# Kernel tuning notes

Hardware: AMD Instinct MI355X
Metric: run time of the kernel (lower is better)

Reference implementation:

```python
import jax, jax.numpy as jnp
import numpy as np

TEMPERATURE = 8.0  # sqrt(d_k)
WINDOW = 2
GATE_THRESH = 0.5
NEG_INF = -1e30


def setup_inputs() -> dict:
    key = jax.random.key(0)
    k1, k2, k3, k4 = jax.random.split(key, 4)
    BH, L, D = 32, 2048, 64
    return {
        "q": jax.random.normal(k1, (BH, L, D), dtype=jnp.float32),
        "k": jax.random.normal(k2, (BH, L, D), dtype=jnp.float32),
        "v": jax.random.normal(k3, (BH, L, D), dtype=jnp.float32),
        "gate_w": jax.random.normal(k4, (1, D), dtype=jnp.float32) * 0.1,
        "gate_b": jnp.zeros((1,), dtype=jnp.float32),
    }


def reference(q, k, v, gate_w, gate_b):
    # q,k: [BH, L, D]; v: [BH, L, Dv]
    BH, Lq, D = q.shape
    Lk = k.shape[1]
    attn = jnp.einsum("bqd,bkd->bqk", q, k) / TEMPERATURE  # [BH, Lq, Lk]
    # per-query gate: if sigmoid(linear(q)) <= thresh, restrict to sliding window
    gate = jax.nn.sigmoid(jnp.einsum("bqd,od->bqo", q, gate_w) + gate_b) > GATE_THRESH  # [BH,Lq,1]
    i = jnp.arange(Lq)[:, None]
    j = jnp.arange(Lk)[None, :]
    window_ok = jnp.abs(i - j) <= WINDOW  # [Lq, Lk]; equals left=max(0,i-W), right=min(Lk,i+W+1)
    allowed = gate | window_ok[None, :, :]  # gate True -> full attention
    attn = jnp.where(allowed, attn, NEG_INF)
    attn = jax.nn.softmax(attn, axis=2)
    # dropout omitted (eval mode)
    out = jnp.einsum("bqk,bkd->bqd", attn, v)
    return out, attn
```

## Files before the change

kernel.cpp:

```cpp
#include <hip/hip_runtime.h>


typedef short bf16x8 __attribute__((ext_vector_type(8)));
typedef float f32x4  __attribute__((ext_vector_type(4)));

#define LSEQ 2048
#define DDIM 64
#define PB_STRIDE 36

__device__ __forceinline__ unsigned short f2bf(float x) {
    unsigned int u = __float_as_uint(x);
    u += 0x7FFFu + ((u >> 16) & 1u);
    return (unsigned short)(u >> 16);
}

__device__ __forceinline__ unsigned int pk2f(float a, float b) {
    return (unsigned int)f2bf(a) | ((unsigned int)f2bf(b) << 16);
}

__device__ __forceinline__ unsigned int pk2u(unsigned short a, unsigned short b) {
    return (unsigned int)a | ((unsigned int)b << 16);
}

__device__ __forceinline__ float pick5(int jj, float e0, float e1, float e2,
                                       float e3, float e4) {
    float r = 0.f;
    r = (jj == 0) ? e0 : r;
    r = (jj == 1) ? e1 : r;
    r = (jj == 2) ? e2 : r;
    r = (jj == 3) ? e3 : r;
    r = (jj == 4) ? e4 : r;
    return r;
}

__global__ __launch_bounds__(256)
void dsa_prep(const float* __restrict__ K, const float* __restrict__ V,
              unsigned short* __restrict__ Kb, unsigned short* __restrict__ Vt)
{
    const int bh  = blockIdx.x >> 5;
    const int k0  = (blockIdx.x & 31) << 6;
    const int tid = threadIdx.x;
    __shared__ unsigned short tileT[64][73];

    const int key = tid >> 2;
    const int d0  = (tid & 3) << 4;
    const float* srcK = K + ((size_t)bh * LSEQ + k0 + key) * DDIM + d0;
    const float* srcV = V + ((size_t)bh * LSEQ + k0 + key) * DDIM + d0;
    {
        uint4 w0, w1;
        w0.x = pk2f(srcK[0],  srcK[1]);  w0.y = pk2f(srcK[2],  srcK[3]);
        w0.z = pk2f(srcK[4],  srcK[5]);  w0.w = pk2f(srcK[6],  srcK[7]);
        w1.x = pk2f(srcK[8],  srcK[9]);  w1.y = pk2f(srcK[10], srcK[11]);
        w1.z = pk2f(srcK[12], srcK[13]); w1.w = pk2f(srcK[14], srcK[15]);
        unsigned short* dst = Kb + ((size_t)bh * LSEQ + k0 + key) * DDIM + d0;
        *(uint4*)(dst)     = w0;
        *(uint4*)(dst + 8) = w1;
    }
    #pragma unroll
    for (int j = 0; j < 16; ++j) tileT[d0 + j][key] = f2bf(srcV[j]);
    __syncthreads();
    {
        const int d   = tid >> 2;
        const int kk0 = (tid & 3) << 4;
        uint4 w0, w1;
        w0.x = pk2u(tileT[d][kk0 + 0],  tileT[d][kk0 + 1]);
        w0.y = pk2u(tileT[d][kk0 + 2],  tileT[d][kk0 + 3]);
        w0.z = pk2u(tileT[d][kk0 + 4],  tileT[d][kk0 + 5]);
        w0.w = pk2u(tileT[d][kk0 + 6],  tileT[d][kk0 + 7]);
        w1.x = pk2u(tileT[d][kk0 + 8],  tileT[d][kk0 + 9]);
        w1.y = pk2u(tileT[d][kk0 + 10], tileT[d][kk0 + 11]);
        w1.z = pk2u(tileT[d][kk0 + 12], tileT[d][kk0 + 13]);
        w1.w = pk2u(tileT[d][kk0 + 14], tileT[d][kk0 + 15]);
        unsigned short* dst = Vt + (size_t)bh * DDIM * LSEQ + (size_t)d * LSEQ + k0 + kk0;
        *(uint4*)(dst)     = w0;
        *(uint4*)(dst + 8) = w1;
    }
}

__global__ __launch_bounds__(256, 4)
void dsa_main(const float* __restrict__ Q,
              const unsigned short* __restrict__ Kb,
              const unsigned short* __restrict__ Vt,
              const float* __restrict__ K32,
              const float* __restrict__ V32,
              const float* __restrict__ GW,
              const float* __restrict__ GB,
              float* __restrict__ OUT,
              float* __restrict__ ATT)
{
    __shared__ float Pbuf[4][16 * PB_STRIDE];
    __shared__ int   sidx[64];
    __shared__ int   gShared;

    const int bx   = blockIdx.x;
    const int bh   = bx >> 5;
    const int q0   = (bx & 31) << 6;
    const int tid  = threadIdx.x;
    const int wave = tid >> 6;
    const int lane = tid & 63;
    const int m16  = lane & 15;
    const int quad = lane >> 4;

    const float* qb = Q + ((size_t)bh * LSEQ + q0) * DDIM;

    if (wave == 0) {
        const float* qr = qb + lane * DDIM;
        float a = 0.f;
        #pragma unroll 8
        for (int d = 0; d < DDIM; ++d) a += qr[d] * GW[d];
        a += GB[0];
        const bool gt = (a > 0.f);
        const unsigned long long b = __ballot(gt);
        const int below = __popcll(b & ((1ull << lane) - 1ull));
        const int g     = __popcll(b);
        const int pos   = gt ? below : (g + (lane - below));
        sidx[pos] = lane;
        if (lane == 0) gShared = g;
    }
    __syncthreads();
    const int g = gShared;
    const int T = (g + 15) >> 4;

    if (wave < T) {
        const unsigned short* kbb = Kb + (size_t)bh * LSEQ * DDIM;
        const unsigned short* vtb = Vt + (size_t)bh * DDIM * LSEQ;
        const int  myIdx = (wave << 4) + m16;
        const bool valid = myIdx < g;
        const int  srow  = sidx[valid ? myIdx : (g - 1)];

        bf16x8 qfrag[2];
        {
            const float* qr = qb + srow * DDIM + (quad << 3);
            #pragma unroll
            for (int db = 0; db < 2; ++db) {
                const float* p = qr + db * 32;
                bf16x8 f;
                #pragma unroll
                for (int j = 0; j < 8; ++j) f[j] = (short)f2bf(p[j]);
                qfrag[db] = f;
            }
        }

        const unsigned short* kp0 = kbb + (size_t)m16 * DDIM + (quad << 3);

        float lsum[4] = {0.f, 0.f, 0.f, 0.f};
        bf16x8 c0 = *(const bf16x8*)(kp0);
        bf16x8 c1 = *(const bf16x8*)(kp0 + 32);
        bf16x8 c2 = *(const bf16x8*)(kp0 + 16 * DDIM);
        bf16x8 c3 = *(const bf16x8*)(kp0 + 16 * DDIM + 32);
        for (int kt = 0; kt < 64; ++kt) {
            const unsigned short* np = kp0 + (size_t)(((kt + 1) & 63) * 32) * DDIM;
            bf16x8 n0 = *(const bf16x8*)(np);
            bf16x8 n1 = *(const bf16x8*)(np + 32);
            bf16x8 n2 = *(const bf16x8*)(np + 16 * DDIM);
            bf16x8 n3 = *(const bf16x8*)(np + 16 * DDIM + 32);
            f32x4 a0 = {0.f, 0.f, 0.f, 0.f}, a1 = {0.f, 0.f, 0.f, 0.f};
            a0 = __builtin_amdgcn_mfma_f32_16x16x32_bf16(qfrag[0], c0, a0, 0, 0, 0);
            a0 = __builtin_amdgcn_mfma_f32_16x16x32_bf16(qfrag[1], c1, a0, 0, 0, 0);
            a1 = __builtin_amdgcn_mfma_f32_16x16x32_bf16(qfrag[0], c2, a1, 0, 0, 0);
            a1 = __builtin_amdgcn_mfma_f32_16x16x32_bf16(qfrag[1], c3, a1, 0, 0, 0);
            #pragma unroll
            for (int r = 0; r < 4; ++r)
                lsum[r] += __expf(a0[r] * 0.125f) + __expf(a1[r] * 0.125f);
            c0 = n0; c1 = n1; c2 = n2; c3 = n3;
        }
        float inv[4];
        #pragma unroll
        for (int r = 0; r < 4; ++r) {
            float x = lsum[r];
            x += __shfl_xor(x, 1); x += __shfl_xor(x, 2);
            x += __shfl_xor(x, 4); x += __shfl_xor(x, 8);
            inv[r] = 1.0f / x;
        }

        f32x4 oacc[4];
        #pragma unroll
        for (int dt = 0; dt < 4; ++dt) oacc[dt] = (f32x4){0.f, 0.f, 0.f, 0.f};
        float* pw  = &Pbuf[wave][0];
        float* ap0 = ATT + ((size_t)(bh * LSEQ + q0 + srow)) * LSEQ + (quad << 3);
        const unsigned short* vp0 = vtb + (size_t)m16 * LSEQ + (quad << 3);

        for (int kt = 0; kt < 64; ++kt) {
            const unsigned short* kp = kp0 + (size_t)(kt * 32) * DDIM;
            bf16x8 k0 = *(const bf16x8*)(kp);
            bf16x8 k1 = *(const bf16x8*)(kp + 32);
            bf16x8 k2 = *(const bf16x8*)(kp + 16 * DDIM);
            bf16x8 k3 = *(const bf16x8*)(kp + 16 * DDIM + 32);
            const unsigned short* vp = vp0 + kt * 32;
            bf16x8 v0 = *(const bf16x8*)(vp);
            bf16x8 v1 = *(const bf16x8*)(vp + 16 * LSEQ);
            bf16x8 v2 = *(const bf16x8*)(vp + 32 * LSEQ);
            bf16x8 v3 = *(const bf16x8*)(vp + 48 * LSEQ);

            f32x4 a0 = {0.f, 0.f, 0.f, 0.f}, a1 = {0.f, 0.f, 0.f, 0.f};
            a0 = __builtin_amdgcn_mfma_f32_16x16x32_bf16(qfrag[0], k0, a0, 0, 0, 0);
            a0 = __builtin_amdgcn_mfma_f32_16x16x32_bf16(qfrag[1], k1, a0, 0, 0, 0);
            a1 = __builtin_amdgcn_mfma_f32_16x16x32_bf16(qfrag[0], k2, a1, 0, 0, 0);
            a1 = __builtin_amdgcn_mfma_f32_16x16x32_bf16(qfrag[1], k3, a1, 0, 0, 0);

            #pragma unroll
            for (int r = 0; r < 4; ++r) {
                const int prow = (quad << 2) + r;
                pw[prow * PB_STRIDE + m16]      = __expf(a0[r] * 0.125f) * inv[r];
                pw[prow * PB_STRIDE + 16 + m16] = __expf(a1[r] * 0.125f) * inv[r];
            }
            const float* prd = pw + m16 * PB_STRIDE + (quad << 3);
            f32x4 p0 = *(const f32x4*)(prd);
            f32x4 p1 = *(const f32x4*)(prd + 4);
            if (valid) {
                float* ap = ap0 + kt * 32;
                *(f32x4*)(ap)     = p0;
                *(f32x4*)(ap + 4) = p1;
            }
            bf16x8 pf;
            #pragma unroll
            for (int j = 0; j < 4; ++j) {
                pf[j]     = (short)f2bf(p0[j]);
                pf[4 + j] = (short)f2bf(p1[j]);
            }
            oacc[0] = __builtin_amdgcn_mfma_f32_16x16x32_bf16(pf, v0, oacc[0], 0, 0, 0);
            oacc[1] = __builtin_amdgcn_mfma_f32_16x16x32_bf16(pf, v1, oacc[1], 0, 0, 0);
            oacc[2] = __builtin_amdgcn_mfma_f32_16x16x32_bf16(pf, v2, oacc[2], 0, 0, 0);
            oacc[3] = __builtin_amdgcn_mfma_f32_16x16x32_bf16(pf, v3, oacc[3], 0, 0, 0);
        }
        #pragma unroll
        for (int r = 0; r < 4; ++r) {
            const int idx = (wave << 4) + (quad << 2) + r;
            if (idx < g) {
                const int orow = sidx[idx];
                float* ob = OUT + ((size_t)(bh * LSEQ + q0 + orow)) * DDIM + m16;
                ob[0]  = oacc[0][r];
                ob[16] = oacc[1][r];
                ob[32] = oacc[2][r];
                ob[48] = oacc[3][r];
            }
        }
    }

    const int nw    = 64 - g;
    const int nww   = (T < 4) ? (4 - T) : 4;
    const int wslot = (T < 4) ? (wave - T) : wave;
    if (wslot >= 0 && nw > 0) {
        for (int ii = wslot; ii < nw; ii += nww) {
            const int row = sidx[g + ii];
            const int i   = q0 + row;
            const float qd = qb[row * DDIM + lane];

            float e[5];
            float denom = 0.f;
            #pragma unroll
            for (int jj = 0; jj < 5; ++jj) {
                const int  j  = i - 2 + jj;
                const bool ok = (j >= 0) && (j < LSEQ);
                const int  jc = ok ? j : 0;
                float t = qd * K32[((size_t)bh * LSEQ + jc) * DDIM + lane];
                t += __shfl_xor(t, 1);  t += __shfl_xor(t, 2);
                t += __shfl_xor(t, 4);  t += __shfl_xor(t, 8);
                t += __shfl_xor(t, 16); t += __shfl_xor(t, 32);
                const float ee = ok ? __expf(t * 0.125f) : 0.f;
                e[jj] = ee;
                denom += ee;
            }
            const float invd = 1.f / denom;
            #pragma unroll
            for (int jj = 0; jj < 5; ++jj) e[jj] *= invd;

            float o = 0.f;
            #pragma unroll
            for (int jj = 0; jj < 5; ++jj) {
                const int  j  = i - 2 + jj;
                const int  jc = (j >= 0 && j < LSEQ) ? j : 0;
                o += e[jj] * V32[((size_t)bh * LSEQ + jc) * DDIM + lane];
            }
            OUT[((size_t)(bh * LSEQ + i)) * DDIM + lane] = o;

            float* ar = ATT + ((size_t)(bh * LSEQ + i)) * LSEQ;
            const int jlo = i - 2;
            #pragma unroll
            for (int it = 0; it < 8; ++it) {
                const int c = (it << 8) + (lane << 2);
                f32x4 z = {0.f, 0.f, 0.f, 0.f};
                if (c + 3 >= jlo && c <= jlo + 4) {
                    #pragma unroll
                    for (int t4 = 0; t4 < 4; ++t4)
                        z[t4] = pick5(c + t4 - jlo, e[0], e[1], e[2], e[3], e[4]);
                }
                *(f32x4*)(ar + c) = z;
            }
        }
    }
}

extern "C" void kernel_launch(void* const* d_in, const int* in_sizes, int n_in,
                              void* d_out, int out_size, void* d_ws, size_t ws_size,
                              hipStream_t stream) {
    const float* q  = (const float*)d_in[0];
    const float* k  = (const float*)d_in[1];
    const float* v  = (const float*)d_in[2];
    const float* gw = (const float*)d_in[3];
    const float* gb = (const float*)d_in[4];

    float* out  = (float*)d_out;
    float* attn = out + (size_t)32 * 2048 * 64;

    unsigned short* Kb = (unsigned short*)d_ws;
    unsigned short* Vt = Kb + (size_t)32 * 2048 * 64;

    dim3 block(256);
    dsa_prep<<<dim3(32 * 32), block, 0, stream>>>(k, v, Kb, Vt);
    dsa_main<<<dim3(32 * 32), block, 0, stream>>>(q, Kb, Vt, k, v, gw, gb, out, attn);
}
```

Before: 792.3 us.

## Split key range across waves for gated rows and reduce partials in LDS

Instead of each wave owning a 16-row tile of gated queries across all 2048 keys, all four waves now cooperate on every tile, each covering a quarter of the keys. Row sums and output partials are combined through shared memory with block barriers. The softmax P buffer is double-buffered, and the windowed rows are spread across all waves afterwards. This targets load imbalance when few tiles exist, at the cost of extra barriers, more LDS, and a dropped occupancy hint in launch bounds.

```diff
diff --git a/kernel.cpp b/kernel.cpp
--- a/kernel.cpp
+++ b/kernel.cpp
@@ -7,6 +7,7 @@
 #define LSEQ 2048
 #define DDIM 64
 #define PB_STRIDE 36
+#define OS_STRIDE 68
 
 __device__ __forceinline__ unsigned short f2bf(float x) {
     unsigned int u = __float_as_uint(x);
@@ -77,7 +78,7 @@
     }
 }
 
-__global__ __launch_bounds__(256, 4)
+__global__ __launch_bounds__(256)
 void dsa_main(const float* __restrict__ Q,
               const unsigned short* __restrict__ Kb,
               const unsigned short* __restrict__ Vt,
@@ -88,7 +89,9 @@
               float* __restrict__ OUT,
               float* __restrict__ ATT)
 {
-    __shared__ float Pbuf[4][16 * PB_STRIDE];
+    __shared__ float Pbuf[4][2][16 * PB_STRIDE];
+    __shared__ float dsum[4][16];
+    __shared__ float osum[4][16][OS_STRIDE];
     __shared__ int   sidx[64];
     __shared__ int   gShared;
 
@@ -112,19 +115,21 @@
         const bool gt = (a > 0.f);
         const unsigned long long b = __ballot(gt);
         const int below = __popcll(b & ((1ull << lane) - 1ull));
-        const int g     = __popcll(b);
-        const int pos   = gt ? below : (g + (lane - below));
+        const int gg    = __popcll(b);
+        const int pos   = gt ? below : (gg + (lane - below));
         sidx[pos] = lane;
-        if (lane == 0) gShared = g;
+        if (lane == 0) gShared = gg;
     }
     __syncthreads();
     const int g = gShared;
     const int T = (g + 15) >> 4;
 
-    if (wave < T) {
-        const unsigned short* kbb = Kb + (size_t)bh * LSEQ * DDIM;
-        const unsigned short* vtb = Vt + (size_t)bh * DDIM * LSEQ;
-        const int  myIdx = (wave << 4) + m16;
+    const unsigned short* kbb = Kb + (size_t)bh * LSEQ * DDIM;
+    const unsigned short* vtb = Vt + (size_t)bh * DDIM * LSEQ;
+    const int kbase = wave << 9;
+
+    for (int t = 0; t < T; ++t) {
+        const int  myIdx = (t << 4) + m16;
         const bool valid = myIdx < g;
         const int  srow  = sidx[valid ? myIdx : (g - 1)];
 
@@ -141,152 +146,172 @@
             }
         }
 
-        const unsigned short* kp0 = kbb + (size_t)m16 * DDIM + (quad << 3);
+        const unsigned short* kp0 = kbb + (size_t)(kbase + m16) * DDIM + (quad << 3);
 
         float lsum[4] = {0.f, 0.f, 0.f, 0.f};
-        bf16x8 c0 = *(const bf16x8*)(kp0);
-        bf16x8 c1 = *(const bf16x8*)(kp0 + 32);
-        bf16x8 c2 = *(const bf16x8*)(kp0 + 16 * DDIM);
-        bf16x8 c3 = *(const bf16x8*)(kp0 + 16 * DDIM + 32);
-        for (int kt = 0; kt < 64; ++kt) {
-            const unsigned short* np = kp0 + (size_t)(((kt + 1) & 63) * 32) * DDIM;
-            bf16x8 n0 = *(const bf16x8*)(np);
-            bf16x8 n1 = *(const bf16x8*)(np + 32);
-            bf16x8 n2 = *(const bf16x8*)(np + 16 * DDIM);
-            bf16x8 n3 = *(const bf16x8*)(np + 16 * DDIM + 32);
-            f32x4 a0 = {0.f, 0.f, 0.f, 0.f}, a1 = {0.f, 0.f, 0.f, 0.f};
-            a0 = __builtin_amdgcn_mfma_f32_16x16x32_bf16(qfrag[0], c0, a0, 0, 0, 0);
-            a0 = __builtin_amdgcn_mfma_f32_16x16x32_bf16(qfrag[1], c1, a0, 0, 0, 0);
-            a1 = __builtin_amdgcn_mfma_f32_16x16x32_bf16(qfrag[0], c2, a1, 0, 0, 0);
-            a1 = __builtin_amdgcn_mfma_f32_16x16x32_bf16(qfrag[1], c3, a1, 0, 0, 0);
-            #pragma unroll
-            for (int r = 0; r < 4; ++r)
-                lsum[r] += __expf(a0[r] * 0.125f) + __expf(a1[r] * 0.125f);
-            c0 = n0; c1 = n1; c2 = n2; c3 = n3;
-        }
-        float inv[4];
-        #pragma unroll
-        for (int r = 0; r < 4; ++r) {
-            float x = lsum[r];
-            x += __shfl_xor(x, 1); x += __shfl_xor(x, 2);
-            x += __shfl_xor(x, 4); x += __shfl_xor(x, 8);
-            inv[r] = 1.0f / x;
-        }
-
-        f32x4 oacc[4];
-        #pragma unroll
-        for (int dt = 0; dt < 4; ++dt) oacc[dt] = (f32x4){0.f, 0.f, 0.f, 0.f};
-        float* pw  = &Pbuf[wave][0];
-        float* ap0 = ATT + ((size_t)(bh * LSEQ + q0 + srow)) * LSEQ + (quad << 3);
-        const unsigned short* vp0 = vtb + (size_t)m16 * LSEQ + (quad << 3);
-
-        for (int kt = 0; kt < 64; ++kt) {
+        for (int kt = 0; kt < 16; ++kt) {
             const unsigned short* kp = kp0 + (size_t)(kt * 32) * DDIM;
             bf16x8 k0 = *(const bf16x8*)(kp);
             bf16x8 k1 = *(const bf16x8*)(kp + 32);
             bf16x8 k2 = *(const bf16x8*)(kp + 16 * DDIM);
             bf16x8 k3 = *(const bf16x8*)(kp + 16 * DDIM + 32);
-            const unsigned short* vp = vp0 + kt * 32;
-            bf16x8 v0 = *(const bf16x8*)(vp);
-            bf16x8 v1 = *(const bf16x8*)(vp + 16 * LSEQ);
-            bf16x8 v2 = *(const bf16x8*)(vp + 32 * LSEQ);
-            bf16x8 v3 = *(const bf16x8*)(vp + 48 * LSEQ);
-
             f32x4 a0 = {0.f, 0.f, 0.f, 0.f}, a1 = {0.f, 0.f, 0.f, 0.f};
             a0 = __builtin_amdgcn_mfma_f32_16x16x32_bf16(qfrag[0], k0, a0, 0, 0, 0);
             a0 = __builtin_amdgcn_mfma_f32_16x16x32_bf16(qfrag[1], k1, a0, 0, 0, 0);
             a1 = __builtin_amdgcn_mfma_f32_16x16x32_bf16(qfrag[0], k2, a1, 0, 0, 0);
             a1 = __builtin_amdgcn_mfma_f32_16x16x32_bf16(qfrag[1], k3, a1, 0, 0, 0);
-
             #pragma unroll
-            for (int r = 0; r < 4; ++r) {
-                const int prow = (quad << 2) + r;
-                pw[prow * PB_STRIDE + m16]      = __expf(a0[r] * 0.125f) * inv[r];
-                pw[prow * PB_STRIDE + 16 + m16] = __expf(a1[r] * 0.125f) * inv[r];
+            for (int r = 0; r < 4; ++r)
+                lsum[r] += __expf(a0[r] * 0.125f) + __expf(a1[r] * 0.125f);
+        }
+        #pragma unroll
+        for (int r = 0; r < 4; ++r) {
+            float x = lsum[r];
+            x += __shfl_xor(x, 1); x += __shfl_xor(x, 2);
+            x += __shfl_xor(x, 4); x += __shfl_xor(x, 8);
+            if (m16 == 0) dsum[wave][(quad << 2) + r] = x;
+        }
+        __syncthreads();
+
+        float inv[4];
+        #pragma unroll
+        for (int r = 0; r < 4; ++r) {
+            const int rr = (quad << 2) + r;
+            inv[r] = 1.0f / (dsum[0][rr] + dsum[1][rr] + dsum[2][rr] + dsum[3][rr]);
+        }
+
+        f32x4 oacc0 = {0.f,0.f,0.f,0.f}, oacc1 = {0.f,0.f,0.f,0.f};
+        f32x4 oacc2 = {0.f,0.f,0.f,0.f}, oacc3 = {0.f,0.f,0.f,0.f};
+        float* ap0 = ATT + ((size_t)(bh * LSEQ + q0 + srow)) * LSEQ + kbase + (quad << 3);
+        const unsigned short* vp0 = vtb + (size_t)m16 * LSEQ + kbase + (quad << 3);
+
+        #define COMPUTE(KT_) {                                                        \
+            const unsigned short* kp = kp0 + (size_t)((KT_) * 32) * DDIM;             \
+            bf16x8 k0 = *(const bf16x8*)(kp);                                         \
+            bf16x8 k1 = *(const bf16x8*)(kp + 32);                                    \
+            bf16x8 k2 = *(const bf16x8*)(kp + 16 * DDIM);                             \
+            bf16x8 k3 = *(const bf16x8*)(kp + 16 * DDIM + 32);                        \
+            f32x4 a0 = {0.f,0.f,0.f,0.f}, a1 = {0.f,0.f,0.f,0.f};                     \
+            a0 = __builtin_amdgcn_mfma_f32_16x16x32_bf16(qfrag[0], k0, a0, 0, 0, 0);  \
+            a0 = __builtin_amdgcn_mfma_f32_16x16x32_bf16(qfrag[1], k1, a0, 0, 0, 0);  \
+            a1 = __builtin_amdgcn_mfma_f32_16x16x32_bf16(qfrag[0], k2, a1, 0, 0, 0);  \
+            a1 = __builtin_amdgcn_mfma_f32_16x16x32_bf16(qfrag[1], k3, a1, 0, 0, 0);  \
+            float* pw = &Pbuf[wave][(KT_) & 1][0];                                    \
+            _Pragma("unroll")                                                         \
+            for (int r = 0; r < 4; ++r) {                                             \
+                const int prow = (quad << 2) + r;                                     \
+                pw[prow * PB_STRIDE + m16]      = __expf(a0[r] * 0.125f) * inv[r];    \
+                pw[prow * PB_STRIDE + 16 + m16] = __expf(a1[r] * 0.125f) * inv[r];    \
+            }                                                                         \
+        }
+
+        #define CONSUME(KT_) {                                                        \
+            const float* prd = &Pbuf[wave][(KT_) & 1][0] + m16 * PB_STRIDE + (quad << 3); \
+            f32x4 p0 = *(const f32x4*)(prd);                                          \
+            f32x4 p1 = *(const f32x4*)(prd + 4);                                      \
+            const unsigned short* vp = vp0 + (KT_) * 32;                              \
+            bf16x8 v0 = *(const bf16x8*)(vp);                                         \
+            bf16x8 v1 = *(const bf16x8*)(vp + 16 * LSEQ);                             \
+            bf16x8 v2 = *(const bf16x8*)(vp + 32 * LSEQ);                             \
+            bf16x8 v3 = *(const bf16x8*)(vp + 48 * LSEQ);                             \
+            if (valid) {                                                              \
+                float* ap = ap0 + (KT_) * 32;                                         \
+                *(f32x4*)(ap)     = p0;                                               \
+                *(f32x4*)(ap + 4) = p1;                                               \
+            }                                                                         \
+            bf16x8 pf;                                                                \
+            _Pragma("unroll")                                                         \
+            for (int j = 0; j < 4; ++j) {                                             \
+                pf[j]     = (short)f2bf(p0[j]);                                       \
+                pf[4 + j] = (short)f2bf(p1[j]);                                       \
+            }                                                                         \
+            oacc0 = __builtin_amdgcn_mfma_f32_16x16x32_bf16(pf, v0, oacc0, 0, 0, 0);  \
+            oacc1 = __builtin_amdgcn_mfma_f32_16x16x32_bf16(pf, v1, oacc1, 0, 0, 0);  \
+            oacc2 = __builtin_amdgcn_mfma_f32_16x16x32_bf16(pf, v2, oacc2, 0, 0, 0);  \
+            oacc3 = __builtin_amdgcn_mfma_f32_16x16x32_bf16(pf, v3, oacc3, 0, 0, 0);  \
+        }
+
+        COMPUTE(0)
+        for (int kt = 1; kt < 16; ++kt) {
+            CONSUME(kt - 1)
+            COMPUTE(kt)
+        }
+        CONSUME(15)
+
+        #undef COMPUTE
+        #undef CONSUME
+
+        #pragma unroll
+        for (int r = 0; r < 4; ++r) {
+            const int prow = (quad << 2) + r;
+            osum[wave][prow][m16]      = oacc0[r];
+            osum[wave][prow][16 + m16] = oacc1[r];
+            osum[wave][prow][32 + m16] = oacc2[r];
+            osum[wave][prow][48 + m16] = oacc3[r];
+        }
+        __syncthreads();
+
+        #pragma unroll
+        for (int rep = 0; rep < 4; ++rep) {
+            const int idx = rep * 256 + tid;
+            const int row = idx >> 6;
+            const int col = idx & 63;
+            const int gi  = (t << 4) + row;
+            if (gi < g) {
+                const float s = osum[0][row][col] + osum[1][row][col]
+                              + osum[2][row][col] + osum[3][row][col];
+                OUT[((size_t)(bh * LSEQ + q0 + sidx[gi])) * DDIM + col] = s;
             }
-            const float* prd = pw + m16 * PB_STRIDE + (quad << 3);
-            f32x4 p0 = *(const f32x4*)(prd);
-            f32x4 p1 = *(const f32x4*)(prd + 4);
-            if (valid) {
-                float* ap = ap0 + kt * 32;
-                *(f32x4*)(ap)     = p0;
-                *(f32x4*)(ap + 4) = p1;
+        }
+        __syncthreads();
+    }
+
+    const int nw = 64 - g;
+    for (int ii = wave; ii < nw; ii += 4) {
+        const int row = sidx[g + ii];
+        const int i   = q0 + row;
+        const float qd = qb[row * DDIM + lane];
+
+        float e[5];
+        float denom = 0.f;
+        #pragma unroll
+        for (int jj = 0; jj < 5; ++jj) {
+            const int  j  = i - 2 + jj;
+            const bool ok = (j >= 0) && (j < LSEQ);
+            const int  jc = ok ? j : 0;
+            float tt = qd * K32[((size_t)bh * LSEQ + jc) * DDIM + lane];
+            tt += __shfl_xor(tt, 1);  tt += __shfl_xor(tt, 2);
+            tt += __shfl_xor(tt, 4);  tt += __shfl_xor(tt, 8);
+            tt += __shfl_xor(tt, 16); tt += __shfl_xor(tt, 32);
+            const float ee = ok ? __expf(tt * 0.125f) : 0.f;
+            e[jj] = ee;
+            denom += ee;
+        }
+        const float invd = 1.f / denom;
+        #pragma unroll
+        for (int jj = 0; jj < 5; ++jj) e[jj] *= invd;
+
+        float o = 0.f;
+        #pragma unroll
+        for (int jj = 0; jj < 5; ++jj) {
+            const int  j  = i - 2 + jj;
+            const int  jc = (j >= 0 && j < LSEQ) ? j : 0;
+            o += e[jj] * V32[((size_t)bh * LSEQ + jc) * DDIM + lane];
+        }
+        OUT[((size_t)(bh * LSEQ + i)) * DDIM + lane] = o;
+
+        float* ar = ATT + ((size_t)(bh * LSEQ + i)) * LSEQ;
+        const int jlo = i - 2;
+        #pragma unroll
+        for (int it = 0; it < 8; ++it) {
+            const int c = (it << 8) + (lane << 2);
+            f32x4 z = {0.f, 0.f, 0.f, 0.f};
+            if (c + 3 >= jlo && c <= jlo + 4) {
+                #pragma unroll
+                for (int t4 = 0; t4 < 4; ++t4)
+                    z[t4] = pick5(c + t4 - jlo, e[0], e[1], e[2], e[3], e[4]);
             }
-            bf16x8 pf;
-            #pragma unroll
-            for (int j = 0; j < 4; ++j) {
-                pf[j]     = (short)f2bf(p0[j]);
-                pf[4 + j] = (short)f2bf(p1[j]);
-            }
-            oacc[0] = __builtin_amdgcn_mfma_f32_16x16x32_bf16(pf, v0, oacc[0], 0, 0, 0);
-            oacc[1] = __builtin_amdgcn_mfma_f32_16x16x32_bf16(pf, v1, oacc[1], 0, 0, 0);
-            oacc[2] = __builtin_amdgcn_mfma_f32_16x16x32_bf16(pf, v2, oacc[2], 0, 0, 0);
-            oacc[3] = __builtin_amdgcn_mfma_f32_16x16x32_bf16(pf, v3, oacc[3], 0, 0, 0);
-        }
-        #pragma unroll
-        for (int r = 0; r < 4; ++r) {
-            const int idx = (wave << 4) + (quad << 2) + r;
-            if (idx < g) {
-                const int orow = sidx[idx];
-                float* ob = OUT + ((size_t)(bh * LSEQ + q0 + orow)) * DDIM + m16;
-                ob[0]  = oacc[0][r];
-                ob[16] = oacc[1][r];
-                ob[32] = oacc[2][r];
-                ob[48] = oacc[3][r];
-            }
-        }
-    }
-
-    const int nw    = 64 - g;
-    const int nww   = (T < 4) ? (4 - T) : 4;
-    const int wslot = (T < 4) ? (wave - T) : wave;
-    if (wslot >= 0 && nw > 0) {
-        for (int ii = wslot; ii < nw; ii += nww) {
-            const int row = sidx[g + ii];
-            const int i   = q0 + row;
-            const float qd = qb[row * DDIM + lane];
-
-            float e[5];
-            float denom = 0.f;
-            #pragma unroll
-            for (int jj = 0; jj < 5; ++jj) {
-                const int  j  = i - 2 + jj;
-                const bool ok = (j >= 0) && (j < LSEQ);
-                const int  jc = ok ? j : 0;
-                float t = qd * K32[((size_t)bh * LSEQ + jc) * DDIM + lane];
-                t += __shfl_xor(t, 1);  t += __shfl_xor(t, 2);
-                t += __shfl_xor(t, 4);  t += __shfl_xor(t, 8);
-                t += __shfl_xor(t, 16); t += __shfl_xor(t, 32);
-                const float ee = ok ? __expf(t * 0.125f) : 0.f;
-                e[jj] = ee;
-                denom += ee;
-            }
-            const float invd = 1.f / denom;
-            #pragma unroll
-            for (int jj = 0; jj < 5; ++jj) e[jj] *= invd;
-
-            float o = 0.f;
-            #pragma unroll
-            for (int jj = 0; jj < 5; ++jj) {
-                const int  j  = i - 2 + jj;
-                const int  jc = (j >= 0 && j < LSEQ) ? j : 0;
-                o += e[jj] * V32[((size_t)bh * LSEQ + jc) * DDIM + lane];
-            }
-            OUT[((size_t)(bh * LSEQ + i)) * DDIM + lane] = o;
-
-            float* ar = ATT + ((size_t)(bh * LSEQ + i)) * LSEQ;
-            const int jlo = i - 2;
-            #pragma unroll
-            for (int it = 0; it < 8; ++it) {
-                const int c = (it << 8) + (lane << 2);
-                f32x4 z = {0.f, 0.f, 0.f, 0.f};
-                if (c + 3 >= jlo && c <= jlo + 4) {
-                    #pragma unroll
-                    for (int t4 = 0; t4 < 4; ++t4)
-                        z[t4] = pick5(c + t4 - jlo, e[0], e[1], e[2], e[3], e[4]);
-                }
-                *(f32x4*)(ar + c) = z;
-            }
+            *(f32x4*)(ar + c) = z;
         }
     }
 }
```

Result: slower. 869.4 us (+9.7%).
